# Performance work log

Measured on AMD Instinct MI355X. Metric: run time of the kernel, lower is better.

The kernel has to match this reference:

```python
import jax, jax.numpy as jnp
import numpy as np

N_DRUG, N_TARGET, N_EDGES, H = 50000, 20000, 500000, 256


def setup_inputs() -> dict:
    key = jax.random.key(0)
    ks = jax.random.split(key, 6)
    s = 1.0 / np.sqrt(2 * H)
    return {
        "z_drug": jax.random.normal(ks[0], (N_DRUG, H), dtype=jnp.float32),
        "z_target": jax.random.normal(ks[1], (N_TARGET, H), dtype=jnp.float32),
        "row": jax.random.randint(ks[2], (N_EDGES,), 0, N_DRUG, dtype=jnp.int64),
        "col": jax.random.randint(ks[3], (N_EDGES,), 0, N_TARGET, dtype=jnp.int64),
        "W1": jax.random.normal(ks[4], (2 * H, H), dtype=jnp.float32) * s,
        "b1": jnp.zeros((H,), dtype=jnp.float32),
        "W2": jax.random.normal(ks[5], (H, 1), dtype=jnp.float32) * (1.0 / np.sqrt(H)),
        "b2": jnp.zeros((1,), dtype=jnp.float32),
    }


def reference(z_drug, z_target, row, col, W1, b1, W2, b2):
    # gather endpoint embeddings by edge index, concat -> [E, 2H]
    zc = jnp.concatenate([z_drug[row], z_target[col]], axis=-1)
    h = jax.nn.relu(zc @ W1 + b1)          # [E, H]
    return h @ W2 + b2                     # [E, 1]
```

## Files before the change

### kernel.cpp

```cpp
#include <hip/hip_runtime.h>
#include <hip/hip_bf16.h>
#include <stdint.h>


typedef unsigned short u16;
typedef __attribute__((ext_vector_type(8))) short short8;
typedef __attribute__((ext_vector_type(4))) float f32x4;

#define HDIM 256
#define KDIM 512
#define BM 128
#define BK 64
#define NWAVE 4

__device__ __forceinline__ u16 f2bf(float f) {
  union { float f; uint32_t u; } v; v.f = f;
  uint32_t u = v.u;
  return (u16)((u + 0x7fffu + ((u >> 16) & 1u)) >> 16);
}

__device__ __forceinline__ void gl2lds16(const void* g, void* l) {
  __builtin_amdgcn_global_load_lds(
      (const __attribute__((address_space(1))) unsigned int*)g,
      (__attribute__((address_space(3))) unsigned int*)l,
      16, 0, 0);
}

#define CVT_BLOCKS 4096
__global__ void prep_kernel(const float* __restrict__ zd_f,
                            const float* __restrict__ zt_f,
                            const float* __restrict__ w1,
                            u16* __restrict__ zdb, u16* __restrict__ ztb,
                            u16* __restrict__ w1t, int n4d, int n4t) {
  const int b = blockIdx.x;
  if (b < 32) {
    __shared__ float tile[64][65];
    const int k0 = (b >> 2) * 64, n0 = (b & 3) * 64;
    const int tx = threadIdx.x & 63, ty = threadIdx.x >> 6;
#pragma unroll
    for (int i = ty; i < 64; i += 4)
      tile[i][tx] = w1[(size_t)(k0 + i) * HDIM + n0 + tx];
    __syncthreads();
#pragma unroll
    for (int i = ty; i < 64; i += 4)
      w1t[(size_t)(n0 + i) * KDIM + k0 + tx] = f2bf(tile[tx][i]);
  } else {
    const int idx = (b - 32) * 256 + threadIdx.x;
    const int stride = CVT_BLOCKS * 256;
    for (int i = idx; i < n4d; i += stride) {
      float4 v = ((const float4*)zd_f)[i];
      ushort4 o; o.x = f2bf(v.x); o.y = f2bf(v.y); o.z = f2bf(v.z); o.w = f2bf(v.w);
      ((ushort4*)zdb)[i] = o;
    }
    for (int i = idx; i < n4t; i += stride) {
      float4 v = ((const float4*)zt_f)[i];
      ushort4 o; o.x = f2bf(v.x); o.y = f2bf(v.y); o.z = f2bf(v.z); o.w = f2bf(v.w);
      ((ushort4*)ztb)[i] = o;
    }
  }
}

__global__ __launch_bounds__(256, 2) void edge_mlp_kernel(
    const u16* __restrict__ zd, const u16* __restrict__ zt,
    const int* __restrict__ row, const int* __restrict__ col,
    const u16* __restrict__ w1t, const float* __restrict__ b1,
    const float* __restrict__ w2, const float* __restrict__ b2,
    float* __restrict__ out, int E) {
  __shared__ u16 lA[2][BM * BK];
  __shared__ float lP[NWAVE * BM];

  const int tid  = threadIdx.x;
  const int wid  = tid >> 6;
  const int lane = tid & 63;
  const int e0   = blockIdx.x * BM;
  const int r8   = lane >> 3;
  const int slog = ((lane & 7) ^ (r8 & 7)) * 8;

  uint32_t offD[4], offT[4];
#pragma unroll
  for (int t = 0; t < 4; ++t) {
    int ge = min(e0 + wid * 32 + r8 + 8 * t, E - 1);
    offD[t] = (uint32_t)row[ge] * HDIM;
    offT[t] = (uint32_t)col[ge] * HDIM;
  }

  f32x4 acc[8][4];
#pragma unroll
  for (int i = 0; i < 8; ++i)
#pragma unroll
    for (int j = 0; j < 4; ++j) acc[i][j] = f32x4{0.f, 0.f, 0.f, 0.f};

  const int colid = lane & 15;
  const int quad  = lane >> 4;
  const int csw   = colid & 7;

  const u16* pW = w1t + (size_t)(wid * 64 + colid) * KDIM + quad * 8;

  auto stage = [&](int kc, int buf) {
    const int koff = (kc & 3) * BK;
    const u16* zbase = (kc < 4) ? zd : zt;
    u16* dA = &lA[buf][(wid * 32) * BK];
#pragma unroll
    for (int t = 0; t < 4; ++t) {
      uint32_t o = (kc < 4) ? offD[t] : offT[t];
      gl2lds16(zbase + o + koff + slog, dA + (8 * t) * BK);
    }
  };

  stage(0, 0);
  asm volatile("s_waitcnt vmcnt(0)" ::: "memory");
  __builtin_amdgcn_s_barrier();

  for (int kc = 0; kc < 8; ++kc) {
    const int cur = kc & 1;

    short8 bF0[4], bF1[4];
#pragma unroll
    for (int ct = 0; ct < 4; ++ct)
      bF0[ct] = *(const short8*)(pW + ct * 16 * KDIM + kc * BK);
#pragma unroll
    for (int ct = 0; ct < 4; ++ct)
      bF1[ct] = *(const short8*)(pW + ct * 16 * KDIM + kc * BK + 32);

    if (kc < 7) stage(kc + 1, cur ^ 1);

    const u16* A = lA[cur];
#pragma unroll
    for (int ks = 0; ks < BK; ks += 32) {
      const int sl = (ks >> 3) + quad;
      short8 aF[8];
#pragma unroll
      for (int rt = 0; rt < 8; ++rt)
        aF[rt] = *(const short8*)&A[(rt * 16 + colid) * BK + ((sl ^ csw) * 8)];
      const short8* bF = (ks == 0) ? bF0 : bF1;
      __builtin_amdgcn_s_setprio(1);
#pragma unroll
      for (int rt = 0; rt < 8; ++rt)
#pragma unroll
        for (int ct = 0; ct < 4; ++ct)
          acc[rt][ct] = __builtin_amdgcn_mfma_f32_16x16x32_bf16(
              aF[rt], bF[ct], acc[rt][ct], 0, 0, 0);
      __builtin_amdgcn_s_setprio(0);
    }
    asm volatile("s_waitcnt vmcnt(0)" ::: "memory");
    __builtin_amdgcn_s_barrier();
  }

  float b1v[4], w2v[4];
#pragma unroll
  for (int ct = 0; ct < 4; ++ct) {
    int n = wid * 64 + ct * 16 + colid;
    b1v[ct] = b1[n];
    w2v[ct] = w2[n];
  }
#pragma unroll
  for (int rt = 0; rt < 8; ++rt)
#pragma unroll
    for (int j = 0; j < 4; ++j) {
      float s = 0.f;
#pragma unroll
      for (int ct = 0; ct < 4; ++ct)
        s += fmaxf(acc[rt][ct][j] + b1v[ct], 0.f) * w2v[ct];
#pragma unroll
      for (int off = 8; off >= 1; off >>= 1)
        s += __shfl_xor(s, off, 16);
      if (colid == 0)
        lP[wid * BM + rt * 16 + quad * 4 + j] = s;
    }
  __syncthreads();
  if (tid < BM) {
    int ge = e0 + tid;
    if (ge < E)
      out[ge] = lP[tid] + lP[BM + tid] + lP[2 * BM + tid] + lP[3 * BM + tid]
                + b2[0];
  }
}

__global__ void fallback_kernel(
    const float* __restrict__ zd, const float* __restrict__ zt,
    const int* __restrict__ row, const int* __restrict__ col,
    const float* __restrict__ W1, const float* __restrict__ b1,
    const float* __restrict__ W2, const float* __restrict__ b2,
    float* __restrict__ out, int E) {
  __shared__ float zc[16][512];
  __shared__ float red[4][16];
  const int e0 = blockIdx.x * 16;
  const int tid = threadIdx.x;
  for (int i = tid; i < 16 * 512; i += 256) {
    int e = i >> 9, k = i & 511;
    int ge = min(e0 + e, E - 1);
    zc[e][k] = (k < HDIM) ? zd[(size_t)row[ge] * HDIM + k]
                          : zt[(size_t)col[ge] * HDIM + (k - HDIM)];
  }
  __syncthreads();
  float acc[16];
#pragma unroll
  for (int e = 0; e < 16; ++e) acc[e] = 0.f;
  for (int k = 0; k < KDIM; ++k) {
    float w = W1[k * HDIM + tid];
#pragma unroll
    for (int e = 0; e < 16; ++e) acc[e] += zc[e][k] * w;
  }
  float wv = W2[tid], bv = b1[tid];
  const int lane = tid & 63, wid = tid >> 6;
#pragma unroll
  for (int e = 0; e < 16; ++e) {
    float pv = fmaxf(acc[e] + bv, 0.f) * wv;
#pragma unroll
    for (int off = 32; off >= 1; off >>= 1) pv += __shfl_down(pv, off, 64);
    if (lane == 0) red[wid][e] = pv;
  }
  __syncthreads();
  if (tid < 16) {
    int ge = e0 + tid;
    if (ge < E)
      out[ge] = red[0][tid] + red[1][tid] + red[2][tid] + red[3][tid] + b2[0];
  }
}

extern "C" void kernel_launch(void* const* d_in, const int* in_sizes, int n_in,
                              void* d_out, int out_size, void* d_ws, size_t ws_size,
                              hipStream_t stream) {
  const float* zd_f = (const float*)d_in[0];
  const float* zt_f = (const float*)d_in[1];
  const int*   row  = (const int*)d_in[2];
  const int*   col  = (const int*)d_in[3];
  const float* W1   = (const float*)d_in[4];
  const float* b1   = (const float*)d_in[5];
  const float* W2   = (const float*)d_in[6];
  const float* b2   = (const float*)d_in[7];
  float* out = (float*)d_out;

  const int E  = in_sizes[2];
  const int ND = in_sizes[0] / HDIM;
  const int NT = in_sizes[1] / HDIM;

  size_t off_w1t = 0;
  size_t off_zd  = (size_t)KDIM * HDIM * sizeof(u16);
  size_t off_zt  = off_zd + (size_t)ND * HDIM * sizeof(u16);
  size_t need    = off_zt + (size_t)NT * HDIM * sizeof(u16);

  if (ws_size >= need) {
    u16* w1t = (u16*)((char*)d_ws + off_w1t);
    u16* zdb = (u16*)((char*)d_ws + off_zd);
    u16* ztb = (u16*)((char*)d_ws + off_zt);
    int n4d = ND * HDIM / 4, n4t = NT * HDIM / 4;
    prep_kernel<<<32 + CVT_BLOCKS, 256, 0, stream>>>(zd_f, zt_f, W1,
                                                     zdb, ztb, w1t, n4d, n4t);
    edge_mlp_kernel<<<(E + BM - 1) / BM, 256, 0, stream>>>(
        zdb, ztb, row, col, w1t, b1, W2, b2, out, E);
  } else {
    fallback_kernel<<<(E + 15) / 16, 256, 0, stream>>>(
        zd_f, zt_f, row, col, W1, b1, W2, b2, out, E);
  }
}
```

Measured before the change: 304.8 us.

## Triple-buffer LDS pipeline with W1 staged through LDS and halved K-chunk

Halves the K chunk to 32 and switches the LDS ring from double to triple buffering, prefetching two chunks ahead with a partial vmcnt wait instead of draining all loads every iteration. The W1 B-fragments are now brought in with async global-to-LDS loads alongside the gathered A rows, instead of per-wave direct global register loads. The swizzle is reworked for the 64-byte rows. The aim is to hide gather and weight-load latency behind MFMA work. The cost is twice as many barriers, extra LDS footprint that may reduce occupancy, and extra LDS reads for B.

```diff
diff --git a/kernel.cpp b/kernel.cpp
--- a/kernel.cpp
+++ b/kernel.cpp
@@ -10,7 +10,8 @@
 #define HDIM 256
 #define KDIM 512
 #define BM 128
-#define BK 64
+#define BK 32
+#define NCH 16
 #define NWAVE 4
 
 __device__ __forceinline__ u16 f2bf(float f) {
@@ -66,23 +67,29 @@
     const u16* __restrict__ w1t, const float* __restrict__ b1,
     const float* __restrict__ w2, const float* __restrict__ b2,
     float* __restrict__ out, int E) {
-  __shared__ u16 lA[2][BM * BK];
+  __shared__ u16 lA[3][BM * BK];
+  __shared__ u16 lB[3][HDIM * BK];
   __shared__ float lP[NWAVE * BM];
 
-  const int tid  = threadIdx.x;
-  const int wid  = tid >> 6;
-  const int lane = tid & 63;
-  const int e0   = blockIdx.x * BM;
-  const int r8   = lane >> 3;
-  const int slog = ((lane & 7) ^ (r8 & 7)) * 8;
-
-  uint32_t offD[4], offT[4];
-#pragma unroll
-  for (int t = 0; t < 4; ++t) {
-    int ge = min(e0 + wid * 32 + r8 + 8 * t, E - 1);
+  const int tid   = threadIdx.x;
+  const int wid   = tid >> 6;
+  const int lane  = tid & 63;
+  const int e0    = blockIdx.x * BM;
+  const int le    = lane >> 2;
+  const int ls    = lane & 3;
+  const int sp    = (ls ^ (le & 3)) * 8;
+  const int colid = lane & 15;
+  const int quad  = lane >> 4;
+  const int cq    = colid & 3;
+
+  uint32_t offD[2], offT[2];
+#pragma unroll
+  for (int t = 0; t < 2; ++t) {
+    int ge = min(e0 + wid * 32 + t * 16 + le, E - 1);
     offD[t] = (uint32_t)row[ge] * HDIM;
     offT[t] = (uint32_t)col[ge] * HDIM;
   }
+  const u16* pB = w1t + (uint32_t)(wid * 64 + le) * KDIM + sp;
 
   f32x4 acc[8][4];
 #pragma unroll
@@ -90,60 +97,56 @@
 #pragma unroll
     for (int j = 0; j < 4; ++j) acc[i][j] = f32x4{0.f, 0.f, 0.f, 0.f};
 
-  const int colid = lane & 15;
-  const int quad  = lane >> 4;
-  const int csw   = colid & 7;
-
-  const u16* pW = w1t + (size_t)(wid * 64 + colid) * KDIM + quad * 8;
-
   auto stage = [&](int kc, int buf) {
-    const int koff = (kc & 3) * BK;
-    const u16* zbase = (kc < 4) ? zd : zt;
-    u16* dA = &lA[buf][(wid * 32) * BK];
-#pragma unroll
-    for (int t = 0; t < 4; ++t) {
-      uint32_t o = (kc < 4) ? offD[t] : offT[t];
-      gl2lds16(zbase + o + koff + slog, dA + (8 * t) * BK);
-    }
+    const u16* zb = (kc < 8) ? zd : zt;
+    const uint32_t* offs = (kc < 8) ? offD : offT;
+    const int koff = (kc & 7) * BK;
+#pragma unroll
+    for (int t = 0; t < 2; ++t)
+      gl2lds16(zb + offs[t] + koff + sp,
+               &lA[buf][(wid * 32 + t * 16) * BK]);
+#pragma unroll
+    for (int t = 0; t < 4; ++t)
+      gl2lds16(pB + (size_t)(t * 16) * KDIM + kc * BK,
+               &lB[buf][(wid * 64 + t * 16) * BK]);
   };
 
   stage(0, 0);
-  asm volatile("s_waitcnt vmcnt(0)" ::: "memory");
+  stage(1, 1);
+  asm volatile("s_waitcnt vmcnt(6)" ::: "memory");
   __builtin_amdgcn_s_barrier();
 
-  for (int kc = 0; kc < 8; ++kc) {
-    const int cur = kc & 1;
-
-    short8 bF0[4], bF1[4];
+#pragma unroll
+  for (int kc = 0; kc < NCH; ++kc) {
+    const int cur = kc % 3;
+    if (kc < NCH - 2) stage(kc + 2, (kc + 2) % 3);
+
+    short8 aF[8], bF[4];
+#pragma unroll
+    for (int rt = 0; rt < 8; ++rt)
+      aF[rt] = *(const short8*)
+          &lA[cur][(rt * 16 + colid) * BK + ((quad ^ cq) * 8)];
 #pragma unroll
     for (int ct = 0; ct < 4; ++ct)
-      bF0[ct] = *(const short8*)(pW + ct * 16 * KDIM + kc * BK);
-#pragma unroll
-    for (int ct = 0; ct < 4; ++ct)
-      bF1[ct] = *(const short8*)(pW + ct * 16 * KDIM + kc * BK + 32);
-
-    if (kc < 7) stage(kc + 1, cur ^ 1);
-
-    const u16* A = lA[cur];
-#pragma unroll
-    for (int ks = 0; ks < BK; ks += 32) {
-      const int sl = (ks >> 3) + quad;
-      short8 aF[8];
-#pragma unroll
-      for (int rt = 0; rt < 8; ++rt)
-        aF[rt] = *(const short8*)&A[(rt * 16 + colid) * BK + ((sl ^ csw) * 8)];
-      const short8* bF = (ks == 0) ? bF0 : bF1;
-      __builtin_amdgcn_s_setprio(1);
-#pragma unroll
-      for (int rt = 0; rt < 8; ++rt)
-#pragma unroll
-        for (int ct = 0; ct < 4; ++ct)
-          acc[rt][ct] = __builtin_amdgcn_mfma_f32_16x16x32_bf16(
-              aF[rt], bF[ct], acc[rt][ct], 0, 0, 0);
-      __builtin_amdgcn_s_setprio(0);
-    }
-    asm volatile("s_waitcnt vmcnt(0)" ::: "memory");
-    __builtin_amdgcn_s_barrier();
+      bF[ct] = *(const short8*)
+          &lB[cur][(wid * 64 + ct * 16 + colid) * BK + ((quad ^ cq) * 8)];
+
+    __builtin_amdgcn_s_setprio(1);
+#pragma unroll
+    for (int rt = 0; rt < 8; ++rt)
+#pragma unroll
+      for (int ct = 0; ct < 4; ++ct)
+        acc[rt][ct] = __builtin_amdgcn_mfma_f32_16x16x32_bf16(
+            aF[rt], bF[ct], acc[rt][ct], 0, 0, 0);
+    __builtin_amdgcn_s_setprio(0);
+
+    if (kc < NCH - 1) {
+      if (kc < NCH - 2)
+        asm volatile("s_waitcnt vmcnt(6)" ::: "memory");
+      else
+        asm volatile("s_waitcnt vmcnt(0)" ::: "memory");
+      __builtin_amdgcn_s_barrier();
+    }
   }
 
   float b1v[4], w2v[4];
```

New measurement: 297.6 us. 2.4% less time.

## Stage W1 tiles through LDS via async global-to-LDS loads with swizzle

Applied to the files above, without the earlier changes.

W1 B-fragments were previously read straight from global memory into registers on every k-chunk. They are now copied asynchronously into a single-buffered, XOR-swizzled LDS tile using global_load_lds, alongside the A gather. Fragments are then read from LDS, and an extra barrier protects the tile before the next chunk overwrites it. The k loop is also fully unrolled. The aim is coalesced, asynchronous W1 traffic that overlaps compute, at the cost of 32KB more LDS per block, which could lower occupancy, and one more barrier per iteration.

```diff
diff --git a/kernel.cpp b/kernel.cpp
--- a/kernel.cpp
+++ b/kernel.cpp
@@ -67,14 +67,18 @@
     const float* __restrict__ w2, const float* __restrict__ b2,
     float* __restrict__ out, int E) {
   __shared__ u16 lA[2][BM * BK];
+  __shared__ u16 lB[HDIM * BK];
   __shared__ float lP[NWAVE * BM];
 
-  const int tid  = threadIdx.x;
-  const int wid  = tid >> 6;
-  const int lane = tid & 63;
-  const int e0   = blockIdx.x * BM;
-  const int r8   = lane >> 3;
-  const int slog = ((lane & 7) ^ (r8 & 7)) * 8;
+  const int tid   = threadIdx.x;
+  const int wid   = tid >> 6;
+  const int lane  = tid & 63;
+  const int e0    = blockIdx.x * BM;
+  const int r8    = lane >> 3;
+  const int slog  = ((lane & 7) ^ (r8 & 7)) * 8;
+  const int colid = lane & 15;
+  const int quad  = lane >> 4;
+  const int csw   = colid & 7;
 
   uint32_t offD[4], offT[4];
 #pragma unroll
@@ -83,6 +87,11 @@
     offD[t] = (uint32_t)row[ge] * HDIM;
     offT[t] = (uint32_t)col[ge] * HDIM;
   }
+  const u16* pB = w1t + (uint32_t)(wid * 64 + r8) * KDIM + slog;
+
+  u16* lAw0 = &lA[0][(wid * 32) * BK];
+  u16* lAw1 = &lA[1][(wid * 32) * BK];
+  u16* lBw  = &lB[(wid * 64) * BK];
 
   f32x4 acc[8][4];
 #pragma unroll
@@ -90,60 +99,70 @@
 #pragma unroll
     for (int j = 0; j < 4; ++j) acc[i][j] = f32x4{0.f, 0.f, 0.f, 0.f};
 
-  const int colid = lane & 15;
-  const int quad  = lane >> 4;
-  const int csw   = colid & 7;
-
-  const u16* pW = w1t + (size_t)(wid * 64 + colid) * KDIM + quad * 8;
-
-  auto stage = [&](int kc, int buf) {
+  auto stageA = [&](int kc, int buf) {
+    const u16* zb = (kc < 4) ? zd : zt;
+    const uint32_t* offs = (kc < 4) ? offD : offT;
     const int koff = (kc & 3) * BK;
-    const u16* zbase = (kc < 4) ? zd : zt;
-    u16* dA = &lA[buf][(wid * 32) * BK];
-#pragma unroll
-    for (int t = 0; t < 4; ++t) {
-      uint32_t o = (kc < 4) ? offD[t] : offT[t];
-      gl2lds16(zbase + o + koff + slog, dA + (8 * t) * BK);
-    }
+    u16* dA = buf ? lAw1 : lAw0;
+#pragma unroll
+    for (int t = 0; t < 4; ++t)
+      gl2lds16(zb + offs[t] + koff + slog, dA + (8 * t) * BK);
   };
-
-  stage(0, 0);
+  auto stageB = [&](int kc) {
+#pragma unroll
+    for (int j = 0; j < 8; ++j)
+      gl2lds16(pB + (size_t)j * 8 * KDIM + kc * BK, lBw + j * 8 * BK);
+  };
+
+  stageA(0, 0);
+  stageB(0);
   asm volatile("s_waitcnt vmcnt(0)" ::: "memory");
   __builtin_amdgcn_s_barrier();
 
+#pragma unroll
   for (int kc = 0; kc < 8; ++kc) {
     const int cur = kc & 1;
 
-    short8 bF0[4], bF1[4];
-#pragma unroll
-    for (int ct = 0; ct < 4; ++ct)
-      bF0[ct] = *(const short8*)(pW + ct * 16 * KDIM + kc * BK);
-#pragma unroll
-    for (int ct = 0; ct < 4; ++ct)
-      bF1[ct] = *(const short8*)(pW + ct * 16 * KDIM + kc * BK + 32);
-
-    if (kc < 7) stage(kc + 1, cur ^ 1);
-
-    const u16* A = lA[cur];
-#pragma unroll
-    for (int ks = 0; ks < BK; ks += 32) {
-      const int sl = (ks >> 3) + quad;
+    short8 bF[2][4];
+#pragma unroll
+    for (int s = 0; s < 2; ++s) {
+      const int sl = s * 4 + quad;
+#pragma unroll
+      for (int ct = 0; ct < 4; ++ct)
+        bF[s][ct] = *(const short8*)
+            &lB[(wid * 64 + ct * 16 + colid) * BK + ((sl ^ csw) * 8)];
+    }
+    asm volatile("s_waitcnt lgkmcnt(0)" ::: "memory");
+    __builtin_amdgcn_s_barrier();
+    __builtin_amdgcn_sched_barrier(0);
+
+    if (kc < 7) {
+      stageA(kc + 1, cur ^ 1);
+      stageB(kc + 1);
+    }
+
+    const u16* A = cur ? (lA[1]) : (lA[0]);
+#pragma unroll
+    for (int s = 0; s < 2; ++s) {
+      const int sl = s * 4 + quad;
       short8 aF[8];
 #pragma unroll
       for (int rt = 0; rt < 8; ++rt)
         aF[rt] = *(const short8*)&A[(rt * 16 + colid) * BK + ((sl ^ csw) * 8)];
-      const short8* bF = (ks == 0) ? bF0 : bF1;
       __builtin_amdgcn_s_setprio(1);
 #pragma unroll
       for (int rt = 0; rt < 8; ++rt)
 #pragma unroll
         for (int ct = 0; ct < 4; ++ct)
           acc[rt][ct] = __builtin_amdgcn_mfma_f32_16x16x32_bf16(
-              aF[rt], bF[ct], acc[rt][ct], 0, 0, 0);
+              aF[rt], bF[s][ct], acc[rt][ct], 0, 0, 0);
       __builtin_amdgcn_s_setprio(0);
     }
-    asm volatile("s_waitcnt vmcnt(0)" ::: "memory");
-    __builtin_amdgcn_s_barrier();
+
+    if (kc < 7) {
+      asm volatile("s_waitcnt vmcnt(0)" ::: "memory");
+      __builtin_amdgcn_s_barrier();
+    }
   }
 
   float b1v[4], w2v[4];
```

Measured after the change: 278.9 us. -8.5%, faster.
